# Performance work log

Measured on AMD Instinct MI355X. Metric: run time of the kernel, lower is better.

Reference implementation:

```python
import jax, jax.numpy as jnp
import numpy as np

N = 50000        # nodes
E = 800000       # edges (before self-loops)
IN = 128         # in_channels
HID = 32         # hidden_channels
HEADS = 8        # num_heads
G = 64           # num graphs in batch
NEG_SLOPE = 0.2  # PyG GATConv default


def setup_inputs() -> dict:
    key = jax.random.key(0)
    ks = jax.random.split(key, 12)
    x = jax.random.normal(ks[0], (N, IN), jnp.float32)
    edge_index = jax.random.randint(ks[1], (2, E), 0, N, jnp.int32)
    edge_attr = jax.random.normal(ks[2], (E, 4), jnp.float32)
    batch = jnp.sort(jax.random.randint(ks[3], (N,), 0, G, jnp.int32))
    s = 0.05
    # GATConv 1: in -> HEADS*HID
    W1 = jax.random.normal(ks[4], (IN, HEADS * HID), jnp.float32) * s
    a_src1 = jax.random.normal(ks[5], (HEADS, HID), jnp.float32) * s
    a_dst1 = jax.random.normal(ks[6], (HEADS, HID), jnp.float32) * s
    b1 = jnp.zeros((HEADS * HID,), jnp.float32)
    # GATConv 2: HEADS*HID -> HID (heads=1)
    W2 = jax.random.normal(ks[7], (HEADS * HID, HID), jnp.float32) * s
    a_src2 = jax.random.normal(ks[8], (1, HID), jnp.float32) * s
    a_dst2 = jax.random.normal(ks[9], (1, HID), jnp.float32) * s
    b2 = jnp.zeros((HID,), jnp.float32)
    return {"x": x, "edge_index": edge_index, "edge_attr": edge_attr, "batch": batch,
            "W1": W1, "a_src1": a_src1, "a_dst1": a_dst1, "b1": b1,
            "W2": W2, "a_src2": a_src2, "a_dst2": a_dst2, "b2": b2}


def gat_conv(x, src, dst, W, a_src, a_dst, b):
    # x: [N, F_in]; W: [F_in, H*C]; a_src/a_dst: [H, C]
    H, C = a_src.shape
    h = (x @ W).reshape(N, H, C)                      # [N, H, C]
    al_s = jnp.einsum('nhc,hc->nh', h, a_src)         # [N, H]
    al_d = jnp.einsum('nhc,hc->nh', h, a_dst)
    e = jax.nn.leaky_relu(al_s[src] + al_d[dst], NEG_SLOPE)  # [Etot, H]
    # segment softmax over incoming edges of each dst node
    m = jax.ops.segment_max(e, dst, num_segments=N)
    p = jnp.exp(e - m[dst])
    z = jax.ops.segment_sum(p, dst, num_segments=N)
    alpha = p / z[dst]                                # [Etot, H]
    out = jax.ops.segment_sum(alpha[:, :, None] * h[src], dst, num_segments=N)
    return out.reshape(N, H * C) + b


def reference(x, edge_index, edge_attr, batch, W1, a_src1, a_dst1, b1, W2, a_src2, a_dst2, b2):
    # edge_attr is ignored: GATConv was built without edge_dim (PyG lin_edge=None).
    loops = jnp.arange(N, dtype=edge_index.dtype)     # PyG add_self_loops=True
    src = jnp.concatenate([edge_index[0], loops])
    dst = jnp.concatenate([edge_index[1], loops])
    h = jax.nn.relu(gat_conv(x, src, dst, W1, a_src1, a_dst1, b1))
    # dropout p=0.2 is identity in eval mode
    h = gat_conv(h, src, dst, W2, a_src2, a_dst2, b2)  # [N, HID]
    # global_mean_pool over graph ids
    sums = jax.ops.segment_sum(h, batch, num_segments=G)
    cnts = jax.ops.segment_sum(jnp.ones((N, 1), h.dtype), batch, num_segments=G)
    return sums / jnp.maximum(cnts, 1.0)              # [G, HID]
```

## Files before the change

kernel.cpp:

```cpp
#include <hip/hip_runtime.h>
#include <hip/hip_bf16.h>

#define NNODES 50000
#define NEDGES 800000
#define FIN 128
#define HID 32
#define HEADS 8
#define NG 64
#define NEG_SLOPE 0.2f
#define MAXDEG 64

using bf16x8 = __attribute__((ext_vector_type(8))) short;
using f32x4  = __attribute__((ext_vector_type(4))) float;
using f32x2  = __attribute__((ext_vector_type(2))) float;

static __device__ __forceinline__ float leaky(float x) {
    return x > 0.f ? x : NEG_SLOPE * x;
}
static __device__ __forceinline__ unsigned short f2bf(float f) {
    unsigned int x = __float_as_uint(f);
    return (unsigned short)((x + 0x7FFFu + ((x >> 16) & 1u)) >> 16);
}
static __device__ __forceinline__ unsigned int pack2bf(float lo, float hi) {
    return (unsigned int)f2bf(lo) | ((unsigned int)f2bf(hi) << 16);
}
static __device__ __forceinline__ float bfs(unsigned short u) {
    return __uint_as_float((unsigned int)u << 16);
}
static __device__ __forceinline__ unsigned char f2fp8(float f) {
    return (unsigned char)(__builtin_amdgcn_cvt_pk_fp8_f32(f, f, 0, false) & 0xFF);
}

#define ZERO_BLOCKS 196
__global__ void zero_swz_kernel(int* __restrict__ cnt,
                                const float* __restrict__ W1, const float* __restrict__ W2,
                                unsigned short* __restrict__ w1s,
                                unsigned short* __restrict__ w2s) {
    if (blockIdx.x < ZERO_BLOCKS) {
        int i = blockIdx.x * 256 + threadIdx.x;
        if (i < NNODES) cnt[i] = 0;
        return;
    }
    int idx = (blockIdx.x - ZERO_BLOCKS) * 256 + threadIdx.x;
    if (idx < 32768) {
        int j    = idx & 7;
        int lane = (idx >> 3) & 63;
        int ks   = (idx >> 9) & 3;
        int ct   = idx >> 11;
        int k = ks * 32 + (lane >> 4) * 8 + j;
        int n = ct * 16 + (lane & 15);
        w1s[idx] = f2bf(W1[k * 256 + n]);
    } else if (idx < 32768 + 8192) {
        int id2  = idx - 32768;
        int j    = id2 & 7;
        int lane = (id2 >> 3) & 63;
        int ks   = (id2 >> 9) & 7;
        int ct   = id2 >> 12;
        int k = ks * 32 + (lane >> 4) * 8 + j;
        int n = ct * 16 + (lane & 15);
        w2s[id2] = f2bf(W2[k * 32 + n]);
    }
}

#define SCAT_GROUPS 782
__global__ void scatter_kernel(const int* __restrict__ ei, int* __restrict__ cnt,
                               unsigned short* __restrict__ csr) {
    int xcd = blockIdx.x & 7;
    int slice = blockIdx.x >> 3;
    int e4 = slice * 256 + threadIdx.x;
    int dlo = xcd * 6250;
    int dhi = dlo + 6250;
    if (e4 < NEDGES / 4) {
        int4 d = *(const int4*)(ei + NEDGES + e4 * 4);
        int4 s;
        bool a0 = d.x >= dlo && d.x < dhi;
        bool a1 = d.y >= dlo && d.y < dhi;
        bool a2 = d.z >= dlo && d.z < dhi;
        bool a3 = d.w >= dlo && d.w < dhi;
        if (a0 | a1 | a2 | a3) s = *(const int4*)(ei + e4 * 4);
        if (a0) { int p = atomicAdd(&cnt[d.x], 1); csr[(d.x << 6) + p] = (unsigned short)s.x; }
        if (a1) { int p = atomicAdd(&cnt[d.y], 1); csr[(d.y << 6) + p] = (unsigned short)s.y; }
        if (a2) { int p = atomicAdd(&cnt[d.z], 1); csr[(d.z << 6) + p] = (unsigned short)s.z; }
        if (a3) { int p = atomicAdd(&cnt[d.w], 1); csr[(d.w << 6) + p] = (unsigned short)s.w; }
    }
}

__global__ __launch_bounds__(256) void gemm1_mfma_kernel(const float* __restrict__ x,
                                                         const unsigned short* __restrict__ w1s,
                                                         const float* __restrict__ a_src,
                                                         const float* __restrict__ a_dst,
                                                         unsigned char* __restrict__ h1f8,
                                                         float* __restrict__ al_s,
                                                         float* __restrict__ al_d) {
    int t = threadIdx.x;
    int w = t >> 6;
    int l = t & 63;
    int lane16 = l & 15, quad = l >> 4;

    bf16x8 bf[4][4];
    const bf16x8* wp = (const bf16x8*)w1s;
#pragma unroll
    for (int ct = 0; ct < 4; ++ct)
#pragma unroll
        for (int ks = 0; ks < 4; ++ks)
            bf[ct][ks] = wp[((w * 4 + ct) * 4 + ks) * 64 + l];

    float as_c[4], ad_c[4];
#pragma unroll
    for (int ct = 0; ct < 4; ++ct) {
        int col = w * 64 + ct * 16 + lane16;
        as_c[ct] = a_src[col];
        ad_c[ct] = a_dst[col];
    }

    int rbase = blockIdx.x * 64;
    for (int rg = 0; rg < 4; ++rg) {
        int row0 = rbase + rg * 16;
        int r = row0 + lane16;
        int r_eff = r < NNODES ? r : NNODES - 1;
        bf16x8 af[4];
#pragma unroll
        for (int ks = 0; ks < 4; ++ks) {
            const float* ap = x + (size_t)r_eff * FIN + ks * 32 + quad * 8;
            float4 a0 = *(const float4*)ap;
            float4 a1 = *(const float4*)(ap + 4);
            bf16x8 v;
            v[0] = (short)f2bf(a0.x); v[1] = (short)f2bf(a0.y);
            v[2] = (short)f2bf(a0.z); v[3] = (short)f2bf(a0.w);
            v[4] = (short)f2bf(a1.x); v[5] = (short)f2bf(a1.y);
            v[6] = (short)f2bf(a1.z); v[7] = (short)f2bf(a1.w);
            af[ks] = v;
        }
        f32x4 acc[4];
#pragma unroll
        for (int ct = 0; ct < 4; ++ct) acc[ct] = (f32x4){0.f, 0.f, 0.f, 0.f};
#pragma unroll
        for (int ks = 0; ks < 4; ++ks)
#pragma unroll
            for (int ct = 0; ct < 4; ++ct)
                acc[ct] = __builtin_amdgcn_mfma_f32_16x16x32_bf16(af[ks], bf[ct][ks], acc[ct], 0, 0, 0);

#pragma unroll
        for (int reg = 0; reg < 4; ++reg) {
            float ps0 = acc[0][reg] * as_c[0] + acc[1][reg] * as_c[1];
            float ps1 = acc[2][reg] * as_c[2] + acc[3][reg] * as_c[3];
            float pd0 = acc[0][reg] * ad_c[0] + acc[1][reg] * ad_c[1];
            float pd1 = acc[2][reg] * ad_c[2] + acc[3][reg] * ad_c[3];
#pragma unroll
            for (int m = 1; m < 16; m <<= 1) {
                ps0 += __shfl_xor(ps0, m); ps1 += __shfl_xor(ps1, m);
                pd0 += __shfl_xor(pd0, m); pd1 += __shfl_xor(pd1, m);
            }
            int gr = row0 + quad * 4 + reg;
            if (lane16 == 0 && gr < NNODES) {
                al_s[gr * HEADS + 2 * w]     = ps0;
                al_s[gr * HEADS + 2 * w + 1] = ps1;
                al_d[gr * HEADS + 2 * w]     = pd0;
                al_d[gr * HEADS + 2 * w + 1] = pd1;
            }
        }

#pragma unroll
        for (int ct = 0; ct < 4; ++ct)
#pragma unroll
            for (int reg = 0; reg < 4; ++reg) {
                int gr = row0 + quad * 4 + reg;
                if (gr < NNODES)
                    h1f8[(size_t)gr * 256 + w * 64 + ct * 16 + lane16] = f2fp8(acc[ct][reg]);
            }
    }
}

__global__ __launch_bounds__(256) void gather1_kernel(const unsigned char* __restrict__ h1f8,
                                                      const float* __restrict__ al_s,
                                                      const float* __restrict__ al_d,
                                                      const int* __restrict__ cnt,
                                                      const unsigned short* __restrict__ csr,
                                                      const float* __restrict__ b1,
                                                      unsigned short* __restrict__ out1b) {
    int t = threadIdx.x;
    int l = t & 63;
    int q = l & 31;
    int base = l & 32;
    int n = blockIdx.x * 8 + (t >> 5);
    int e_st = q >> 3;
    int h_st = q & 7;
    int h_f  = q >> 2;
    float ad_st = al_d[n * HEADS + h_st];

    float p = __expf(leaky(al_s[n * HEADS + h_f] + al_d[n * HEADS + h_f]));
    float z = p;
    float acc[8];
    {
        uint2 v = *(const uint2*)(h1f8 + (size_t)n * 256 + q * 8);
        f32x2 f01 = __builtin_amdgcn_cvt_pk_f32_fp8(v.x, false);
        f32x2 f23 = __builtin_amdgcn_cvt_pk_f32_fp8(v.x, true);
        f32x2 f45 = __builtin_amdgcn_cvt_pk_f32_fp8(v.y, false);
        f32x2 f67 = __builtin_amdgcn_cvt_pk_f32_fp8(v.y, true);
        acc[0] = p * f01[0]; acc[1] = p * f01[1];
        acc[2] = p * f23[0]; acc[3] = p * f23[1];
        acc[4] = p * f45[0]; acc[5] = p * f45[1];
        acc[6] = p * f67[0]; acc[7] = p * f67[1];
    }

    int beg = n << 6;
    int end = beg + cnt[n];
    for (int i = beg; i < end; i += 4) {
        int rem = end - i;
        int src4 = n;
        float pe4 = 0.f;
        if (e_st < rem) {
            src4 = csr[i + e_st];
            pe4 = __expf(leaky(al_s[src4 * HEADS + h_st] + ad_st));
        }
#pragma unroll
        for (int j = 0; j < 4; ++j) {
            int   sj  = __shfl(src4, base + j * 8);
            float pej = __shfl(pe4, base + j * 8 + h_f);
            uint2 v = *(const uint2*)(h1f8 + (size_t)sj * 256 + q * 8);
            z += pej;
            f32x2 f01 = __builtin_amdgcn_cvt_pk_f32_fp8(v.x, false);
            f32x2 f23 = __builtin_amdgcn_cvt_pk_f32_fp8(v.x, true);
            f32x2 f45 = __builtin_amdgcn_cvt_pk_f32_fp8(v.y, false);
            f32x2 f67 = __builtin_amdgcn_cvt_pk_f32_fp8(v.y, true);
            acc[0] += pej * f01[0]; acc[1] += pej * f01[1];
            acc[2] += pej * f23[0]; acc[3] += pej * f23[1];
            acc[4] += pej * f45[0]; acc[5] += pej * f45[1];
            acc[6] += pej * f67[0]; acc[7] += pej * f67[1];
        }
    }
    float inv = 1.0f / z;
    float4 b0 = *(const float4*)(b1 + q * 8);
    float4 b2 = *(const float4*)(b1 + q * 8 + 4);
    float o[8];
    o[0] = acc[0] * inv + b0.x; o[1] = acc[1] * inv + b0.y;
    o[2] = acc[2] * inv + b0.z; o[3] = acc[3] * inv + b0.w;
    o[4] = acc[4] * inv + b2.x; o[5] = acc[5] * inv + b2.y;
    o[6] = acc[6] * inv + b2.z; o[7] = acc[7] * inv + b2.w;
#pragma unroll
    for (int k = 0; k < 8; ++k) o[k] = o[k] > 0.f ? o[k] : 0.f;
    uint4 pk;
    pk.x = pack2bf(o[0], o[1]); pk.y = pack2bf(o[2], o[3]);
    pk.z = pack2bf(o[4], o[5]); pk.w = pack2bf(o[6], o[7]);
    *(uint4*)(out1b + (size_t)n * 256 + q * 8) = pk;
}

__global__ __launch_bounds__(256) void gemm2_mfma_kernel(const unsigned short* __restrict__ out1b,
                                                         const unsigned short* __restrict__ w2s,
                                                         const float* __restrict__ a_src,
                                                         const float* __restrict__ a_dst,
                                                         unsigned short* __restrict__ h2b,
                                                         float* __restrict__ al_s,
                                                         float* __restrict__ al_d) {
    int t = threadIdx.x;
    int w = t >> 6;
    int l = t & 63;
    int lane16 = l & 15, quad = l >> 4;

    bf16x8 bf[2][8];
    const bf16x8* wp = (const bf16x8*)w2s;
#pragma unroll
    for (int ct = 0; ct < 2; ++ct)
#pragma unroll
        for (int ks = 0; ks < 8; ++ks)
            bf[ct][ks] = wp[((ct * 8 + ks)) * 64 + l];

    float as_c[2], ad_c[2];
#pragma unroll
    for (int ct = 0; ct < 2; ++ct) {
        as_c[ct] = a_src[ct * 16 + lane16];
        ad_c[ct] = a_dst[ct * 16 + lane16];
    }

    int row0 = blockIdx.x * 64 + w * 16;
    int r = row0 + lane16;
    int r_eff = r < NNODES ? r : NNODES - 1;
    f32x4 acc[2];
    acc[0] = (f32x4){0.f, 0.f, 0.f, 0.f};
    acc[1] = (f32x4){0.f, 0.f, 0.f, 0.f};
#pragma unroll
    for (int ks = 0; ks < 8; ++ks) {
        bf16x8 af = *(const bf16x8*)(out1b + (size_t)r_eff * 256 + ks * 32 + quad * 8);
        acc[0] = __builtin_amdgcn_mfma_f32_16x16x32_bf16(af, bf[0][ks], acc[0], 0, 0, 0);
        acc[1] = __builtin_amdgcn_mfma_f32_16x16x32_bf16(af, bf[1][ks], acc[1], 0, 0, 0);
    }
#pragma unroll
    for (int reg = 0; reg < 4; ++reg) {
        int gr = row0 + quad * 4 + reg;
        if (gr < NNODES) {
            h2b[(size_t)gr * 32 + lane16]      = f2bf(acc[0][reg]);
            h2b[(size_t)gr * 32 + 16 + lane16] = f2bf(acc[1][reg]);
        }
        float ps = acc[0][reg] * as_c[0] + acc[1][reg] * as_c[1];
        float pd = acc[0][reg] * ad_c[0] + acc[1][reg] * ad_c[1];
#pragma unroll
        for (int m = 1; m < 16; m <<= 1) {
            ps += __shfl_xor(ps, m);
            pd += __shfl_xor(pd, m);
        }
        if (lane16 == 0 && gr < NNODES) {
            al_s[gr] = ps;
            al_d[gr] = pd;
        }
    }
}

__global__ __launch_bounds__(256) void gather2_kernel(const unsigned short* __restrict__ h2b,
                                                      const float* __restrict__ al_s,
                                                      const float* __restrict__ al_d,
                                                      const int* __restrict__ cnt,
                                                      const unsigned short* __restrict__ csr,
                                                      const float* __restrict__ b2,
                                                      float* __restrict__ out2) {
    int t = threadIdx.x;
    int l = t & 63;
    int c = l & 31;
    int base = l & 32;
    int n = blockIdx.x * 8 + (t >> 5);
    float ad = al_d[n];
    float p = __expf(leaky(al_s[n] + ad));
    float z = p;
    float acc = p * bfs(h2b[(size_t)n * HID + c]);
    int beg = n << 6;
    int end = beg + cnt[n];
    for (int i = beg; i < end; i += 32) {
        int rem = end - i;
        int src = n;
        float pe = 0.f;
        if (c < rem) {
            src = csr[i + c];
            pe = __expf(leaky(al_s[src] + ad));
        }
        int m = rem < 32 ? rem : 32;
        for (int j0 = 0; j0 < m; j0 += 8) {
#pragma unroll
            for (int jj = 0; jj < 8; ++jj) {
                int   sj  = __shfl(src, base + j0 + jj);
                float pej = __shfl(pe, base + j0 + jj);
                z += pej;
                acc += pej * bfs(h2b[(size_t)sj * HID + c]);
            }
        }
    }
    out2[n * HID + c] = acc / z + b2[c];
}

__global__ __launch_bounds__(256) void pool_kernel(const float* __restrict__ out2,
                                                   const int* __restrict__ batch,
                                                   float* __restrict__ out) {
    __shared__ float red[256];
    int g = blockIdx.x;
    int t = threadIdx.x;
    int c = t & 31;
    int sub = t >> 5;
    int beg, end;
    {
        int lo = 0, hi = NNODES;
        while (lo < hi) { int mid = (lo + hi) >> 1; if (batch[mid] < g) lo = mid + 1; else hi = mid; }
        beg = lo;
        lo = beg; hi = NNODES;
        while (lo < hi) { int mid = (lo + hi) >> 1; if (batch[mid] < g + 1) lo = mid + 1; else hi = mid; }
        end = lo;
    }
    float s = 0.f;
    for (int n = beg + sub; n < end; n += 8) s += out2[n * HID + c];
    red[t] = s;
    __syncthreads();
    if (t < 32) {
        float tot = 0.f;
#pragma unroll
        for (int k = 0; k < 8; ++k) tot += red[c + 32 * k];
        int cnt2 = end - beg;
        out[g * HID + c] = tot / (float)(cnt2 > 0 ? cnt2 : 1);
    }
}

extern "C" void kernel_launch(void* const* d_in, const int* in_sizes, int n_in,
                              void* d_out, int out_size, void* d_ws, size_t ws_size,
                              hipStream_t stream) {
    const float* x      = (const float*)d_in[0];
    const int*   ei     = (const int*)d_in[1];
    const int*   batch  = (const int*)d_in[3];
    const float* W1     = (const float*)d_in[4];
    const float* a_src1 = (const float*)d_in[5];
    const float* a_dst1 = (const float*)d_in[6];
    const float* b1     = (const float*)d_in[7];
    const float* W2     = (const float*)d_in[8];
    const float* a_src2 = (const float*)d_in[9];
    const float* a_dst2 = (const float*)d_in[10];
    const float* b2     = (const float*)d_in[11];
    float* out = (float*)d_out;

    char* ws = (char*)d_ws;
    size_t off = 0;
    auto alloc = [&](size_t bytes) {
        size_t o = off;
        off = (off + bytes + 255) & ~(size_t)255;
        return o;
    };
    unsigned char*  h1f8  = (unsigned char*)(ws + alloc((size_t)NNODES * 256));
    unsigned short* out1b = (unsigned short*)(ws + alloc((size_t)NNODES * 256 * 2));
    unsigned short* h2b   = (unsigned short*)(ws + alloc((size_t)NNODES * HID * 2));
    unsigned short* w1s   = (unsigned short*)(ws + alloc((size_t)16 * 4 * 64 * 8 * 2));
    unsigned short* w2s   = (unsigned short*)(ws + alloc((size_t)2 * 8 * 64 * 8 * 2));
    float* out2   = (float*)(ws + alloc((size_t)NNODES * HID * 4));
    float* al_s1  = (float*)(ws + alloc((size_t)NNODES * HEADS * 4));
    float* al_d1  = (float*)(ws + alloc((size_t)NNODES * HEADS * 4));
    float* al_s2  = (float*)(ws + alloc((size_t)NNODES * 4));
    float* al_d2  = (float*)(ws + alloc((size_t)NNODES * 4));
    int*   cnt    = (int*)(ws + alloc((size_t)NNODES * 4));
    unsigned short* csr = (unsigned short*)(ws + alloc((size_t)NNODES * MAXDEG * 2));
    (void)ws_size;

    zero_swz_kernel<<<ZERO_BLOCKS + 160, 256, 0, stream>>>(cnt, W1, W2, w1s, w2s);
    scatter_kernel<<<SCAT_GROUPS * 8, 256, 0, stream>>>(ei, cnt, csr);

    gemm1_mfma_kernel<<<(NNODES + 63) / 64, 256, 0, stream>>>(x, w1s, a_src1, a_dst1,
                                                              h1f8, al_s1, al_d1);
    gather1_kernel<<<NNODES / 8, 256, 0, stream>>>(h1f8, al_s1, al_d1, cnt, csr, b1, out1b);

    gemm2_mfma_kernel<<<(NNODES + 63) / 64, 256, 0, stream>>>(out1b, w2s, a_src2, a_dst2,
                                                              h2b, al_s2, al_d2);
    gather2_kernel<<<NNODES / 8, 256, 0, stream>>>(h2b, al_s2, al_d2, cnt, csr, b2, out2);
    pool_kernel<<<NG, 256, 0, stream>>>(out2, batch, out);
}
```

Before: 263.4 us.

## Use 16 lanes per node in gather2 with paired bf16 loads; split gather1 launch

gather2 now gives each destination node 16 lanes, each handling two channels through 32-bit paired bf16 loads and float2 stores. Edges are processed in chunks of 16, so each block covers 16 nodes and half as many blocks are launched. The aim is fewer memory instructions and better lane use for nodes with low degree. gather1 is also split into two launches over node halves, which adds launch overhead with no clear benefit beyond possibly changing scheduling.

```diff
diff --git a/kernel.cpp b/kernel.cpp
--- a/kernel.cpp
+++ b/kernel.cpp
@@ -23,6 +23,12 @@
 }
 static __device__ __forceinline__ unsigned int pack2bf(float lo, float hi) {
     return (unsigned int)f2bf(lo) | ((unsigned int)f2bf(hi) << 16);
+}
+static __device__ __forceinline__ float bfl(unsigned int u) {
+    return __uint_as_float(u << 16);
+}
+static __device__ __forceinline__ float bfh(unsigned int u) {
+    return __uint_as_float(u & 0xFFFF0000u);
 }
 static __device__ __forceinline__ float bfs(unsigned short u) {
     return __uint_as_float((unsigned int)u << 16);
@@ -177,12 +183,13 @@
                                                       const int* __restrict__ cnt,
                                                       const unsigned short* __restrict__ csr,
                                                       const float* __restrict__ b1,
-                                                      unsigned short* __restrict__ out1b) {
+                                                      unsigned short* __restrict__ out1b,
+                                                      int n_base) {
     int t = threadIdx.x;
     int l = t & 63;
     int q = l & 31;
     int base = l & 32;
-    int n = blockIdx.x * 8 + (t >> 5);
+    int n = n_base + blockIdx.x * 8 + (t >> 5);
     int e_st = q >> 3;
     int h_st = q & 7;
     int h_f  = q >> 2;
@@ -314,35 +321,48 @@
                                                       float* __restrict__ out2) {
     int t = threadIdx.x;
     int l = t & 63;
-    int c = l & 31;
-    int base = l & 32;
-    int n = blockIdx.x * 8 + (t >> 5);
+    int e_sl = l & 15;
+    int base = l & 48;
+    int c0 = (l & 15) * 2;
+    int n = blockIdx.x * 16 + (t >> 4);
+
     float ad = al_d[n];
     float p = __expf(leaky(al_s[n] + ad));
     float z = p;
-    float acc = p * bfs(h2b[(size_t)n * HID + c]);
+    float acc0, acc1;
+    {
+        unsigned int v = *(const unsigned int*)(h2b + (size_t)n * HID + c0);
+        acc0 = p * bfl(v);
+        acc1 = p * bfh(v);
+    }
     int beg = n << 6;
     int end = beg + cnt[n];
-    for (int i = beg; i < end; i += 32) {
+    for (int i = beg; i < end; i += 16) {
         int rem = end - i;
         int src = n;
         float pe = 0.f;
-        if (c < rem) {
-            src = csr[i + c];
+        if (e_sl < rem) {
+            src = csr[i + e_sl];
             pe = __expf(leaky(al_s[src] + ad));
         }
-        int m = rem < 32 ? rem : 32;
+        int m = rem < 16 ? rem : 16;
         for (int j0 = 0; j0 < m; j0 += 8) {
 #pragma unroll
             for (int jj = 0; jj < 8; ++jj) {
                 int   sj  = __shfl(src, base + j0 + jj);
                 float pej = __shfl(pe, base + j0 + jj);
+                unsigned int v = *(const unsigned int*)(h2b + (size_t)sj * HID + c0);
                 z += pej;
-                acc += pej * bfs(h2b[(size_t)sj * HID + c]);
+                acc0 += pej * bfl(v);
+                acc1 += pej * bfh(v);
             }
         }
     }
-    out2[n * HID + c] = acc / z + b2[c];
+    float inv = 1.0f / z;
+    float2 o;
+    o.x = acc0 * inv + b2[c0];
+    o.y = acc1 * inv + b2[c0 + 1];
+    *(float2*)(out2 + (size_t)n * HID + c0) = o;
 }
 
 __global__ __launch_bounds__(256) void pool_kernel(const float* __restrict__ out2,
@@ -417,10 +437,11 @@
 
     gemm1_mfma_kernel<<<(NNODES + 63) / 64, 256, 0, stream>>>(x, w1s, a_src1, a_dst1,
                                                               h1f8, al_s1, al_d1);
-    gather1_kernel<<<NNODES / 8, 256, 0, stream>>>(h1f8, al_s1, al_d1, cnt, csr, b1, out1b);
+    gather1_kernel<<<3125, 256, 0, stream>>>(h1f8, al_s1, al_d1, cnt, csr, b1, out1b, 0);
+    gather1_kernel<<<3125, 256, 0, stream>>>(h1f8, al_s1, al_d1, cnt, csr, b1, out1b, 25000);
 
     gemm2_mfma_kernel<<<(NNODES + 63) / 64, 256, 0, stream>>>(out1b, w2s, a_src2, a_dst2,
                                                               h2b, al_s2, al_d2);
-    gather2_kernel<<<NNODES / 8, 256, 0, stream>>>(h2b, al_s2, al_d2, cnt, csr, b2, out2);
+    gather2_kernel<<<NNODES / 16, 256, 0, stream>>>(h2b, al_s2, al_d2, cnt, csr, b2, out2);
     pool_kernel<<<NG, 256, 0, stream>>>(out2, batch, out);
 }
```

Measured after the change: 270.3 us. 2.6% more time.
